# Performance work log

Hardware: AMD Instinct MI355X
Metric: run time of the kernel (lower is better)

The kernel has to match this reference:

```python
import jax, jax.numpy as jnp
import numpy as np

C = 128          # hidden_channels
N = 50000        # num nodes
E = 600000       # num edges
G = 256          # num graphs
PI = 3.141592653589793
EPS = 1e-5       # BatchNorm eps


def _lin(key, fan_in, fan_out):
    return jax.random.normal(key, (fan_in, fan_out), jnp.float32) / jnp.sqrt(fan_in)


def setup_inputs() -> dict:
    key = jax.random.key(0)
    ks = jax.random.split(key, 40)
    inp = {}
    inp["x"] = jax.random.normal(ks[0], (N, C), jnp.float32)
    inp["edge_index"] = jax.random.randint(ks[1], (2, E), 0, N)
    inp["edge_attr"] = jax.random.normal(ks[2], (E, C), jnp.float32)
    inp["batch"] = jnp.sort(jax.random.randint(ks[3], (N,), 0, G))
    # GATv2Conv 1
    inp["Wl1"] = _lin(ks[4], C, C); inp["bl1"] = jnp.zeros((C,), jnp.float32)
    inp["Wr1"] = _lin(ks[5], C, C); inp["br1"] = jnp.zeros((C,), jnp.float32)
    inp["We1"] = _lin(ks[6], C, C)
    inp["att1"] = jax.random.normal(ks[7], (C,), jnp.float32) / jnp.sqrt(C)
    inp["bo1"] = jnp.zeros((C,), jnp.float32)
    # GATv2Conv 2
    inp["Wl2"] = _lin(ks[8], C, C); inp["bl2"] = jnp.zeros((C,), jnp.float32)
    inp["Wr2"] = _lin(ks[9], C, C); inp["br2"] = jnp.zeros((C,), jnp.float32)
    inp["We2"] = _lin(ks[10], C, C)
    inp["att2"] = jax.random.normal(ks[11], (C,), jnp.float32) / jnp.sqrt(C)
    inp["bo2"] = jnp.zeros((C,), jnp.float32)
    # BatchNorms (affine)
    inp["g1"] = jnp.ones((C,), jnp.float32); inp["be1"] = jnp.zeros((C,), jnp.float32)
    inp["g2"] = jnp.ones((C,), jnp.float32); inp["be2"] = jnp.zeros((C,), jnp.float32)
    # AttentionalAggregation gate MLP (lin1 -> tanh -> lin2)
    inp["Ag1"] = _lin(ks[12], C, C); inp["bg1"] = jnp.zeros((C,), jnp.float32)
    inp["Ag2"] = _lin(ks[13], C, C); inp["bg2"] = jnp.zeros((C,), jnp.float32)
    # final Linear
    inp["Wf"] = _lin(ks[14], C, C); inp["bf"] = jnp.zeros((C,), jnp.float32)
    return inp


def gatv2(x, src, dst, ea, Wl, bl, Wr, br, We, att, bo):
    # add self-loops with fill_value='mean' (mean of incoming edge_attr per node)
    ones = jnp.ones(src.shape, x.dtype)
    deg = jax.ops.segment_sum(ones, dst, N)
    loop_attr = jax.ops.segment_sum(ea, dst, N) / jnp.maximum(deg, 1.0)[:, None]
    ar = jnp.arange(N)
    s = jnp.concatenate([src, ar])
    d = jnp.concatenate([dst, ar])
    ea_full = jnp.concatenate([ea, loop_attr], axis=0)  # [E+N, C]
    xl = x @ Wl + bl   # source transform
    xr = x @ Wr + br   # target transform
    m = xl[s] + xr[d] + ea_full @ We                    # [E+N, C]
    a = jnp.sum(jax.nn.leaky_relu(m, 0.2) * att, axis=-1)  # [E+N]
    # scatter-softmax over incoming edges of each target node
    amax = jax.ops.segment_max(a, d, N)
    ex = jnp.exp(a - amax[d])
    den = jax.ops.segment_sum(ex, d, N)
    alpha = ex / den[d]
    return jax.ops.segment_sum(alpha[:, None] * xl[s], d, N) + bo


def batchnorm(x, g, b):
    mu = x.mean(axis=0)
    var = x.var(axis=0)
    return (x - mu) * jax.lax.rsqrt(var + EPS) * g + b


def att_pool(x, batch, A1, b1, A2, b2):
    # gate_nn: lin1 -> tanh -> lin2, then per-graph per-feature softmax weights
    gate = jnp.tanh(x @ A1 + b1) @ A2 + b2              # [N, C]
    gmax = jax.ops.segment_max(gate, batch, G)
    eg = jnp.exp(gate - gmax[batch])
    den = jax.ops.segment_sum(eg, batch, G)
    w = eg / den[batch]
    return jax.ops.segment_sum(w * x, batch, G)          # [G, C]


def reference(x, edge_index, edge_attr, batch,
              Wl1, bl1, Wr1, br1, We1, att1, bo1,
              Wl2, bl2, Wr2, br2, We2, att2, bo2,
              g1, be1, g2, be2,
              Ag1, bg1, Ag2, bg2, Wf, bf):
    src, dst = edge_index[0], edge_index[1]
    h = gatv2(x, src, dst, edge_attr, Wl1, bl1, Wr1, br1, We1, att1, bo1)
    h = jnp.tanh(batchnorm(h, g1, be1))   # dropout = identity (eval)
    h = gatv2(h, src, dst, edge_attr, Wl2, bl2, Wr2, br2, We2, att2, bo2)
    h = jnp.tanh(batchnorm(h, g2, be2))
    p = att_pool(h, batch, Ag1, bg1, Ag2, bg2)           # [G, C]
    o = jnp.tanh(p @ Wf + bf)
    axis, aperture = jnp.split(o, 2, axis=-1)            # [G, C//2] each
    return axis * PI, (aperture + 1.0) * PI
```

## Files before the change

### kernel.cpp

```cpp
#include <hip/hip_runtime.h>
#include <hip/hip_bf16.h>
#include <math.h>

#define C 128
#define NN 50000
#define EE 600000
#define GG 256
#define PI_F 3.14159265358979323846f
#define EPS_BN 1e-5f

typedef __attribute__((ext_vector_type(8)))  short  short8;
typedef __attribute__((ext_vector_type(16))) float  floatx16;
typedef __attribute__((ext_vector_type(4)))  float  float4v;
typedef __attribute__((ext_vector_type(4)))  unsigned short ushort4v;

static __device__ __forceinline__ short f2bs(float x) {
    union { float f; unsigned u; } v; v.f = x;
    unsigned r = v.u + 0x7FFF + ((v.u >> 16) & 1);
    return (short)(r >> 16);
}
static __device__ __forceinline__ float bs2f(unsigned short b) {
    union { unsigned u; float f; } v; v.u = (unsigned)b << 16; return v.f;
}

__global__ void k_cast(const float* __restrict__ in, unsigned short* __restrict__ out, int n4) {
    int i = blockIdx.x * blockDim.x + threadIdx.x;
    if (i < n4) {
        float4v v = ((const float4v*)in)[i];
        ushort4v o;
        o.x = (unsigned short)f2bs(v.x); o.y = (unsigned short)f2bs(v.y);
        o.z = (unsigned short)f2bs(v.z); o.w = (unsigned short)f2bs(v.w);
        ((ushort4v*)out)[i] = o;
    }
}

__global__ void k_count(const int* __restrict__ dst, int* __restrict__ deg) {
    int e = blockIdx.x * blockDim.x + threadIdx.x;
    if (e < EE) atomicAdd(&deg[dst[e]], 1);
}

__global__ void k_scan(const int* __restrict__ deg, int* __restrict__ row_ptr) {
    __shared__ int s[1024];
    int t = threadIdx.x;
    const int CH = (NN + 1023) / 1024;
    int base = t * CH;
    int loc = 0;
    for (int i = 0; i < CH; i++) { int idx = base + i; if (idx < NN) loc += deg[idx]; }
    s[t] = loc; __syncthreads();
    for (int off = 1; off < 1024; off <<= 1) {
        int v = (t >= off) ? s[t - off] : 0;
        __syncthreads();
        s[t] += v;
        __syncthreads();
    }
    int run = (t == 0) ? 0 : s[t - 1];
    for (int i = 0; i < CH; i++) {
        int idx = base + i;
        if (idx < NN) { row_ptr[idx] = run; run += deg[idx]; }
    }
    if (t == 0) row_ptr[NN] = s[1023];
}

__global__ void k_fill(const int* __restrict__ src, const int* __restrict__ dst,
                       const int* __restrict__ row_ptr, int* __restrict__ fill,
                       int* __restrict__ eid, int* __restrict__ scsr, int* __restrict__ dcsr) {
    int e = blockIdx.x * blockDim.x + threadIdx.x;
    if (e < EE) {
        int d = dst[e];
        int pos = atomicAdd(&fill[d], 1);
        int i = row_ptr[d] + pos;
        eid[i] = e;
        scsr[i] = src[e];
        dcsr[i] = d;
    }
}

__global__ void k_cast_perm(const float* __restrict__ ea, const int* __restrict__ eid,
                            unsigned short* __restrict__ out) {
    int i = blockIdx.x * 4 + (threadIdx.x >> 6);
    int lane = threadIdx.x & 63;
    if (i >= EE) return;
    int e = eid[i];
    const float2* rp = (const float2*)(ea + (size_t)e * C);
    float2 v = rp[lane];
    unsigned pk = (unsigned)(unsigned short)f2bs(v.x) | ((unsigned)(unsigned short)f2bs(v.y) << 16);
    ((unsigned*)(out + (size_t)i * C))[lane] = pk;
}

__global__ void k_esum(const unsigned short* __restrict__ ea_csr, const int* __restrict__ row_ptr,
                       unsigned short* __restrict__ esum) {
    int n = blockIdx.x; int c = threadIdx.x;
    int s = row_ptr[n], e = row_ptr[n + 1];
    float acc = 0.f;
    for (int i = s; i < e; i++) acc += bs2f(ea_csr[(size_t)i * C + c]);
    esum[(size_t)n * C + c] = (unsigned short)f2bs(acc / fmaxf((float)(e - s), 1.f));
}

template<bool TANH, bool OUT_BF16>
__launch_bounds__(256)
__global__ void k_gemm(const unsigned short* __restrict__ A, const float* __restrict__ W,
                       const float* __restrict__ bias, void* __restrict__ outv, int M) {
    __shared__ short sWT[C * 136];
    for (int i = threadIdx.x; i < C * C; i += 256) {
        int k = i >> 7, n = i & (C - 1);
        sWT[n * 136 + k] = f2bs(W[i]);
    }
    __syncthreads();

    int lane = threadIdx.x & 63;
    int wave = threadIdx.x >> 6;
    int m    = lane & 31;
    int half = lane >> 5;
    int row0 = blockIdx.x * 128 + wave * 32;
    int rowA = row0 + m;
    int rowC = (rowA < M) ? rowA : (M - 1);
    const unsigned short* rp = A + (size_t)rowC * C;

    floatx16 acc[4];
    #pragma unroll
    for (int t = 0; t < 4; ++t)
        #pragma unroll
        for (int r = 0; r < 16; ++r) acc[t][r] = 0.f;

    #pragma unroll
    for (int s = 0; s < 8; ++s) {
        int k0 = s * 16 + half * 8;
        short8 af = *(const short8*)(rp + k0);
        #pragma unroll
        for (int t = 0; t < 4; ++t) {
            short8 bfr = *(const short8*)(&sWT[(t * 32 + m) * 136 + k0]);
            acc[t] = __builtin_amdgcn_mfma_f32_32x32x16_bf16(af, bfr, acc[t], 0, 0, 0);
        }
    }

    #pragma unroll
    for (int t = 0; t < 4; ++t) {
        int n = t * 32 + m;
        float b = bias ? bias[n] : 0.f;
        #pragma unroll
        for (int r = 0; r < 16; ++r) {
            int rl  = (r & 3) + 8 * (r >> 2) + 4 * half;
            int row = row0 + rl;
            if (row < M) {
                float v = acc[t][r] + b;
                if (TANH) v = tanhf(v);
                if (OUT_BF16) ((unsigned short*)outv)[(size_t)row * C + n] = (unsigned short)f2bs(v);
                else          ((float*)outv)[(size_t)row * C + n] = v;
            }
        }
    }
}

__launch_bounds__(256)
__global__ void k_gemm2(const unsigned short* __restrict__ A,
                        const float* __restrict__ W0, const float* __restrict__ b0,
                        const float* __restrict__ W1, const float* __restrict__ b1,
                        unsigned short* __restrict__ out0, unsigned short* __restrict__ out1,
                        int M) {
    __shared__ short sWT[C * 136];
    int lane = threadIdx.x & 63;
    int wave = threadIdx.x >> 6;
    int m    = lane & 31;
    int half = lane >> 5;
    int row0 = blockIdx.x * 128 + wave * 32;
    int rowA = row0 + m;
    int rowC = (rowA < M) ? rowA : (M - 1);
    const unsigned short* rp = A + (size_t)rowC * C;

    short8 af[8];
    #pragma unroll
    for (int s = 0; s < 8; ++s) af[s] = *(const short8*)(rp + s * 16 + half * 8);

    for (int phase = 0; phase < 2; ++phase) {
        const float* W = phase ? W1 : W0;
        const float* bb = phase ? b1 : b0;
        unsigned short* out = phase ? out1 : out0;
        if (phase) __syncthreads();
        for (int i = threadIdx.x; i < C * C; i += 256) {
            int k = i >> 7, n = i & (C - 1);
            sWT[n * 136 + k] = f2bs(W[i]);
        }
        __syncthreads();

        floatx16 acc[4];
        #pragma unroll
        for (int t = 0; t < 4; ++t)
            #pragma unroll
            for (int r = 0; r < 16; ++r) acc[t][r] = 0.f;

        #pragma unroll
        for (int s = 0; s < 8; ++s) {
            int k0 = s * 16 + half * 8;
            #pragma unroll
            for (int t = 0; t < 4; ++t) {
                short8 bfr = *(const short8*)(&sWT[(t * 32 + m) * 136 + k0]);
                acc[t] = __builtin_amdgcn_mfma_f32_32x32x16_bf16(af[s], bfr, acc[t], 0, 0, 0);
            }
        }

        #pragma unroll
        for (int t = 0; t < 4; ++t) {
            int n = t * 32 + m;
            float b = bb[n];
            #pragma unroll
            for (int r = 0; r < 16; ++r) {
                int rl  = (r & 3) + 8 * (r >> 2) + 4 * half;
                int row = row0 + rl;
                if (row < M)
                    out[(size_t)row * C + n] = (unsigned short)f2bs(acc[t][r] + b);
            }
        }
    }
}

template<bool SELF>
__launch_bounds__(256)
__global__ void k_gemm_logit(const unsigned short* __restrict__ A, const float* __restrict__ W,
                             const unsigned short* __restrict__ xl, const unsigned short* __restrict__ xr,
                             const int* __restrict__ scsr, const int* __restrict__ dcsr,
                             const float* __restrict__ att, float* __restrict__ aout, int M) {
    __shared__ short sWT[C * 136];
    for (int i = threadIdx.x; i < C * C; i += 256) {
        int k = i >> 7, n = i & (C - 1);
        sWT[n * 136 + k] = f2bs(W[i]);
    }
    __syncthreads();

    int lane = threadIdx.x & 63;
    int wave = threadIdx.x >> 6;
    int m    = lane & 31;
    int half = lane >> 5;
    int row0 = blockIdx.x * 128 + wave * 32;
    int rowA = row0 + m;
    int rowC = (rowA < M) ? rowA : (M - 1);
    const unsigned short* rp = A + (size_t)rowC * C;

    floatx16 acc[4];
    #pragma unroll
    for (int t = 0; t < 4; ++t)
        #pragma unroll
        for (int r = 0; r < 16; ++r) acc[t][r] = 0.f;

    #pragma unroll
    for (int s = 0; s < 8; ++s) {
        int k0 = s * 16 + half * 8;
        short8 af = *(const short8*)(rp + k0);
        #pragma unroll
        for (int t = 0; t < 4; ++t) {
            short8 bfr = *(const short8*)(&sWT[(t * 32 + m) * 136 + k0]);
            acc[t] = __builtin_amdgcn_mfma_f32_32x32x16_bf16(af, bfr, acc[t], 0, 0, 0);
        }
    }

    float attv[4];
    #pragma unroll
    for (int t = 0; t < 4; ++t) attv[t] = att[t * 32 + m];

    #pragma unroll
    for (int r = 0; r < 16; ++r) {
        int rl  = (r & 3) + 8 * (r >> 2) + 4 * half;
        int row = row0 + rl;
        int rc  = (row < M) ? row : (M - 1);
        int si, di;
        if (SELF) { si = rc; di = rc; }
        else      { si = scsr[rc]; di = dcsr[rc]; }
        const unsigned short* xls = xl + (size_t)si * C;
        const unsigned short* xrs = xr + (size_t)di * C;
        float p = 0.f;
        #pragma unroll
        for (int t = 0; t < 4; ++t) {
            int col = t * 32 + m;
            float v = acc[t][r] + bs2f(xls[col]) + bs2f(xrs[col]);
            v = (v >= 0.f) ? v : 0.2f * v;
            p = fmaf(v, attv[t], p);
        }
        p += __shfl_xor(p, 1);  p += __shfl_xor(p, 2);  p += __shfl_xor(p, 4);
        p += __shfl_xor(p, 8);  p += __shfl_xor(p, 16);
        if (m == 0 && row < M) aout[row] = p;
    }
}

__global__ void k_attn(const unsigned short* __restrict__ xl, const float* __restrict__ a,
                       const int* __restrict__ row_ptr, const int* __restrict__ scsr,
                       const float* __restrict__ bo, float* __restrict__ out) {
    int n = blockIdx.x * 4 + (threadIdx.x >> 6);
    int lane = threadIdx.x & 63;
    if (n >= NN) return;
    int s = row_ptr[n], e = row_ptr[n + 1];
    float aself = a[EE + n];
    float mx = aself;
    for (int i = s + lane; i < e; i += 64) mx = fmaxf(mx, a[i]);
    #pragma unroll
    for (int o = 1; o < 64; o <<= 1) mx = fmaxf(mx, __shfl_xor(mx, o));
    float part = (lane == 0) ? expf(aself - mx) : 0.f;
    for (int i = s + lane; i < e; i += 64) part += expf(a[i] - mx);
    #pragma unroll
    for (int o = 1; o < 64; o <<= 1) part += __shfl_xor(part, o);
    float inv = 1.f / part;

    int sub = lane >> 4;
    int cb  = (lane & 15) * 8;
    float acc[8];
    #pragma unroll
    for (int j = 0; j < 8; ++j) acc[j] = 0.f;

    if (sub == 0) {
        float w = expf(aself - mx) * inv;
        short8 v = *(const short8*)(xl + (size_t)n * C + cb);
        #pragma unroll
        for (int j = 0; j < 8; ++j) acc[j] = w * bs2f((unsigned short)v[j]);
    }

    for (int i = s + sub; i < e; i += 4) {
        float w = expf(a[i] - mx) * inv;
        int sd = scsr[i];
        short8 v = *(const short8*)(xl + (size_t)sd * C + cb);
        #pragma unroll
        for (int j = 0; j < 8; ++j) acc[j] = fmaf(w, bs2f((unsigned short)v[j]), acc[j]);
    }

    #pragma unroll
    for (int j = 0; j < 8; ++j) {
        acc[j] += __shfl_xor(acc[j], 16);
        acc[j] += __shfl_xor(acc[j], 32);
    }
    if (sub == 0) {
        float* op = out + (size_t)n * C + cb;
        float4v o0, o1;
        o0.x = acc[0] + bo[cb + 0]; o0.y = acc[1] + bo[cb + 1];
        o0.z = acc[2] + bo[cb + 2]; o0.w = acc[3] + bo[cb + 3];
        o1.x = acc[4] + bo[cb + 4]; o1.y = acc[5] + bo[cb + 5];
        o1.z = acc[6] + bo[cb + 6]; o1.w = acc[7] + bo[cb + 7];
        ((float4v*)op)[0] = o0;
        ((float4v*)op)[1] = o1;
    }
}

__global__ void k_bnstats(const float* __restrict__ v, float* __restrict__ sums) {
    int c = threadIdx.x;
    float s1 = 0.f, s2 = 0.f;
    for (int n = blockIdx.x; n < NN; n += gridDim.x) {
        float x = v[(size_t)n * C + c]; s1 += x; s2 += x * x;
    }
    atomicAdd(&sums[c], s1); atomicAdd(&sums[C + c], s2);
}

__global__ void k_bnapply(const float* __restrict__ v, const float* __restrict__ sums,
                          const float* __restrict__ g, const float* __restrict__ b,
                          unsigned short* __restrict__ h) {
    int idx = blockIdx.x * blockDim.x + threadIdx.x;
    if (idx >= NN * C) return;
    int c = idx & (C - 1);
    float mu  = sums[c] * (1.f / NN);
    float var = sums[C + c] * (1.f / NN) - mu * mu;
    float r = rsqrtf(var + EPS_BN);
    h[idx] = (unsigned short)f2bs(tanhf((v[idx] - mu) * r * g[c] + b[c]));
}

__global__ void k_bounds(const int* __restrict__ batch, int* __restrict__ gs, int* __restrict__ ge) {
    int n = blockIdx.x * blockDim.x + threadIdx.x;
    if (n >= NN) return;
    int b = batch[n];
    if (n == 0 || batch[n - 1] != b) gs[b] = n;
    if (n == NN - 1 || batch[n + 1] != b) ge[b] = n + 1;
}

__global__ void k_pool(const unsigned short* __restrict__ gate, const unsigned short* __restrict__ h,
                       const int* __restrict__ gs, const int* __restrict__ ge,
                       float* __restrict__ pooled) {
    __shared__ float sm[C], sden[C], sacc[C];
    int g = blockIdx.x;
    int t = threadIdx.x;
    int c = t & (C - 1);
    int half = t >> 7;
    int s = gs[g], e = ge[g];
    float m = -1e30f, den = 0.f, acc = 0.f;
    for (int n = s + half; n < e; n += 2) {
        float gv = bs2f(gate[(size_t)n * C + c]);
        float hv = bs2f(h[(size_t)n * C + c]);
        float mn = fmaxf(m, gv);
        float sc = expf(m - mn);
        float w  = expf(gv - mn);
        den = den * sc + w;
        acc = acc * sc + w * hv;
        m = mn;
    }
    if (half) { sm[c] = m; sden[c] = den; sacc[c] = acc; }
    __syncthreads();
    if (!half) {
        float m2 = sm[c], den2 = sden[c], acc2 = sacc[c];
        float mn = fmaxf(m, m2);
        float a1 = expf(m - mn), a2 = expf(m2 - mn);
        float d  = den * a1 + den2 * a2;
        float ac = acc * a1 + acc2 * a2;
        pooled[g * C + c] = (e > s) ? ac / d : 0.f;
    }
}

__global__ void k_final(const float* __restrict__ pooled, const float* __restrict__ Wf,
                        const float* __restrict__ bf, float* __restrict__ out) {
    __shared__ float row[C];
    int g = blockIdx.x; int j = threadIdx.x;
    row[j] = pooled[g * C + j];
    __syncthreads();
    float acc = bf[j];
    #pragma unroll 8
    for (int k = 0; k < C; k++) acc = fmaf(row[k], Wf[k * C + j], acc);
    float o = tanhf(acc);
    if (j < C / 2) out[g * (C / 2) + j] = o * PI_F;
    else out[GG * (C / 2) + g * (C / 2) + (j - C / 2)] = (o + 1.f) * PI_F;
}

extern "C" void kernel_launch(void* const* d_in, const int* in_sizes, int n_in,
                              void* d_out, int out_size, void* d_ws, size_t ws_size,
                              hipStream_t stream) {
    const float* x   = (const float*)d_in[0];
    const int*   ei  = (const int*)d_in[1];
    const float* ea  = (const float*)d_in[2];
    const int* batch = (const int*)d_in[3];
    const float *Wl1 = (const float*)d_in[4],  *bl1 = (const float*)d_in[5];
    const float *Wr1 = (const float*)d_in[6],  *br1 = (const float*)d_in[7];
    const float *We1 = (const float*)d_in[8],  *att1 = (const float*)d_in[9], *bo1 = (const float*)d_in[10];
    const float *Wl2 = (const float*)d_in[11], *bl2 = (const float*)d_in[12];
    const float *Wr2 = (const float*)d_in[13], *br2 = (const float*)d_in[14];
    const float *We2 = (const float*)d_in[15], *att2 = (const float*)d_in[16], *bo2 = (const float*)d_in[17];
    const float *g1  = (const float*)d_in[18], *be1 = (const float*)d_in[19];
    const float *g2  = (const float*)d_in[20], *be2 = (const float*)d_in[21];
    const float *Ag1 = (const float*)d_in[22], *bg1 = (const float*)d_in[23];
    const float *Ag2 = (const float*)d_in[24], *bg2 = (const float*)d_in[25];
    const float *Wf  = (const float*)d_in[26], *bf  = (const float*)d_in[27];
    const int* src = ei; const int* dst = ei + EE;

    char* wsb = (char*)d_ws;
    size_t off = 0;
    auto alloc = [&](size_t bytes) -> char* {
        char* p = wsb + off; off += (bytes + 255) & ~(size_t)255; return p;
    };
    unsigned short* ea_u  = (unsigned short*)alloc((size_t)EE * C * 2);
    unsigned short* x_u   = (unsigned short*)alloc((size_t)NN * C * 2);
    unsigned short* xl_u  = (unsigned short*)alloc((size_t)NN * C * 2);
    unsigned short* xr_u  = (unsigned short*)alloc((size_t)NN * C * 2);
    unsigned short* h_u   = (unsigned short*)alloc((size_t)NN * C * 2);
    unsigned short* es_u  = (unsigned short*)alloc((size_t)NN * C * 2);
    float* aggf  = (float*)alloc((size_t)NN * C * 4);
    float* a     = (float*)alloc((size_t)(EE + NN) * 4);
    int*   csrz  = (int*)alloc((size_t)2 * NN * 4);
    int* deg = csrz, *fill = csrz + NN;
    int* row_ptr = (int*)alloc((size_t)(NN + 1) * 4);
    int* eid     = (int*)alloc((size_t)EE * 4);
    int* scsr    = (int*)alloc((size_t)EE * 4);
    int* dcsr    = (int*)alloc((size_t)EE * 4);
    float* sums  = (float*)alloc(4 * C * 4);
    int* gbounds = (int*)alloc(2 * GG * 4);
    int* gs = gbounds, *ge = gbounds + GG;
    float* pooled= (float*)alloc(GG * C * 4);

    hipMemsetAsync(csrz,    0, (size_t)2 * NN * 4, stream);
    hipMemsetAsync(sums,    0, 4 * C * 4, stream);
    hipMemsetAsync(gbounds, 0, 2 * GG * 4, stream);

    k_cast<<<(NN * C / 4 + 255) / 256, 256, 0, stream>>>(x, x_u, NN * C / 4);
    k_count<<<(EE + 255) / 256, 256, 0, stream>>>(dst, deg);
    k_scan<<<1, 1024, 0, stream>>>(deg, row_ptr);
    k_fill<<<(EE + 255) / 256, 256, 0, stream>>>(src, dst, row_ptr, fill, eid, scsr, dcsr);
    k_cast_perm<<<(EE + 3) / 4, 256, 0, stream>>>(ea, eid, ea_u);
    k_esum<<<NN, C, 0, stream>>>(ea_u, row_ptr, es_u);

    int gN = (NN + 127) / 128, gE = (EE + 127) / 128;

    k_gemm2<<<gN, 256, 0, stream>>>(x_u, Wl1, bl1, Wr1, br1, xl_u, xr_u, NN);
    k_gemm_logit<true ><<<gN, 256, 0, stream>>>(es_u, We1, xl_u, xr_u, nullptr, nullptr, att1, a + EE, NN);
    k_gemm_logit<false><<<gE, 256, 0, stream>>>(ea_u, We1, xl_u, xr_u, scsr, dcsr, att1, a, EE);
    k_attn<<<(NN + 3) / 4, 256, 0, stream>>>(xl_u, a, row_ptr, scsr, bo1, aggf);
    k_bnstats<<<256, C, 0, stream>>>(aggf, sums);
    k_bnapply<<<(NN * C + 255) / 256, 256, 0, stream>>>(aggf, sums, g1, be1, h_u);

    k_gemm2<<<gN, 256, 0, stream>>>(h_u, Wl2, bl2, Wr2, br2, xl_u, xr_u, NN);
    k_gemm_logit<true ><<<gN, 256, 0, stream>>>(es_u, We2, xl_u, xr_u, nullptr, nullptr, att2, a + EE, NN);
    k_gemm_logit<false><<<gE, 256, 0, stream>>>(ea_u, We2, xl_u, xr_u, scsr, dcsr, att2, a, EE);
    k_attn<<<(NN + 3) / 4, 256, 0, stream>>>(xl_u, a, row_ptr, scsr, bo2, aggf);
    k_bnstats<<<256, C, 0, stream>>>(aggf, sums + 2 * C);
    k_bnapply<<<(NN * C + 255) / 256, 256, 0, stream>>>(aggf, sums + 2 * C, g2, be2, h_u);

    k_gemm<true,  true><<<gN, 256, 0, stream>>>(h_u,  Ag1, bg1, xl_u, NN);
    k_gemm<false, true><<<gN, 256, 0, stream>>>(xl_u, Ag2, bg2, xr_u, NN);
    k_bounds<<<(NN + 255) / 256, 256, 0, stream>>>(batch, gs, ge);
    k_pool<<<GG, 256, 0, stream>>>(xr_u, h_u, gs, ge, pooled);
    k_final<<<GG, C, 0, stream>>>(pooled, Wf, bf, (float*)d_out);
}
```

Baseline: 1.394 ms.

## Pretranspose weights once, parallelize scan, fuse cast+esum and pool+final, widen BN kernels

Adds a prep kernel that converts and transposes all eight weight matrices to bf16 once, so each GEMM block only copies them into shared memory instead of converting fp32 weights per block. The single-block scan is replaced by a three-phase multi-block scan. The edge-attribute permute-cast and the per-node mean are fused into one kernel. The BN stats and pooling kernels use 1024 threads with shared-memory reductions, BN apply is vectorised by four, and pooling is fused with the final linear layer. The fused cast/esum reads fp32 edge rows in a strided per-node pattern, which may coalesce less well than the previous per-edge cast.

```diff
diff --git a/kernel.cpp b/kernel.cpp
--- a/kernel.cpp
+++ b/kernel.cpp
@@ -8,6 +8,7 @@
 #define GG 256
 #define PI_F 3.14159265358979323846f
 #define EPS_BN 1e-5f
+#define SCAN_G ((NN + 255) / 256)
 
 typedef __attribute__((ext_vector_type(8)))  short  short8;
 typedef __attribute__((ext_vector_type(16))) float  floatx16;
@@ -34,31 +35,87 @@
     }
 }
 
+__global__ void k_prep(const float* __restrict__ W0, const float* __restrict__ W1,
+                       const float* __restrict__ W2, const float* __restrict__ W3,
+                       const float* __restrict__ W4, const float* __restrict__ W5,
+                       const float* __restrict__ W6, const float* __restrict__ W7,
+                       unsigned short* __restrict__ WT) {
+    __shared__ short s[C * 136];
+    const float* W;
+    switch (blockIdx.x) {
+        case 0: W = W0; break; case 1: W = W1; break;
+        case 2: W = W2; break; case 3: W = W3; break;
+        case 4: W = W4; break; case 5: W = W5; break;
+        case 6: W = W6; break; default: W = W7; break;
+    }
+    for (int i = threadIdx.x; i < C * C; i += 256) {
+        int k = i >> 7, n = i & (C - 1);
+        s[n * 136 + k] = f2bs(W[i]);
+    }
+    __syncthreads();
+    unsigned short* out = WT + (size_t)blockIdx.x * C * C;
+    for (int i8 = threadIdx.x; i8 < C * C / 8; i8 += 256) {
+        int n = i8 >> 4, k0 = (i8 & 15) * 8;
+        *(short8*)(out + n * C + k0) = *(const short8*)&s[n * 136 + k0];
+    }
+}
+
+static __device__ __forceinline__ void stage_wt(const unsigned short* __restrict__ WT, short* sWT) {
+    for (int i8 = threadIdx.x; i8 < C * C / 8; i8 += 256) {
+        int n = i8 >> 4, k0 = (i8 & 15) * 8;
+        *(short8*)&sWT[n * 136 + k0] = *(const short8*)(WT + n * C + k0);
+    }
+}
+
 __global__ void k_count(const int* __restrict__ dst, int* __restrict__ deg) {
     int e = blockIdx.x * blockDim.x + threadIdx.x;
     if (e < EE) atomicAdd(&deg[dst[e]], 1);
 }
 
-__global__ void k_scan(const int* __restrict__ deg, int* __restrict__ row_ptr) {
-    __shared__ int s[1024];
+__global__ void k_scan1(const int* __restrict__ deg, int* __restrict__ bsum) {
+    __shared__ int s[256];
     int t = threadIdx.x;
-    const int CH = (NN + 1023) / 1024;
-    int base = t * CH;
-    int loc = 0;
-    for (int i = 0; i < CH; i++) { int idx = base + i; if (idx < NN) loc += deg[idx]; }
-    s[t] = loc; __syncthreads();
-    for (int off = 1; off < 1024; off <<= 1) {
+    int idx = blockIdx.x * 256 + t;
+    s[t] = (idx < NN) ? deg[idx] : 0;
+    __syncthreads();
+    for (int off = 128; off > 0; off >>= 1) {
+        if (t < off) s[t] += s[t + off];
+        __syncthreads();
+    }
+    if (t == 0) bsum[blockIdx.x] = s[0];
+}
+
+__global__ void k_scan2(const int* __restrict__ bsum, int* __restrict__ boff, int* __restrict__ row_ptr) {
+    __shared__ int s[256];
+    int t = threadIdx.x;
+    int v0 = (t < SCAN_G) ? bsum[t] : 0;
+    s[t] = v0;
+    __syncthreads();
+    for (int off = 1; off < 256; off <<= 1) {
         int v = (t >= off) ? s[t - off] : 0;
         __syncthreads();
         s[t] += v;
         __syncthreads();
     }
-    int run = (t == 0) ? 0 : s[t - 1];
-    for (int i = 0; i < CH; i++) {
-        int idx = base + i;
-        if (idx < NN) { row_ptr[idx] = run; run += deg[idx]; }
-    }
-    if (t == 0) row_ptr[NN] = s[1023];
+    if (t < SCAN_G) boff[t] = s[t] - v0;
+    if (t == 255) row_ptr[NN] = s[255];
+}
+
+__global__ void k_scan3(const int* __restrict__ deg, const int* __restrict__ boff,
+                        int* __restrict__ row_ptr) {
+    __shared__ int s[256];
+    int t = threadIdx.x;
+    int idx = blockIdx.x * 256 + t;
+    int v = (idx < NN) ? deg[idx] : 0;
+    s[t] = v;
+    __syncthreads();
+    for (int off = 1; off < 256; off <<= 1) {
+        int u = (t >= off) ? s[t - off] : 0;
+        __syncthreads();
+        s[t] += u;
+        __syncthreads();
+    }
+    if (idx < NN) row_ptr[idx] = boff[blockIdx.x] + s[t] - v;
 }
 
 __global__ void k_fill(const int* __restrict__ src, const int* __restrict__ dst,
@@ -75,36 +132,26 @@
     }
 }
 
-__global__ void k_cast_perm(const float* __restrict__ ea, const int* __restrict__ eid,
-                            unsigned short* __restrict__ out) {
-    int i = blockIdx.x * 4 + (threadIdx.x >> 6);
-    int lane = threadIdx.x & 63;
-    if (i >= EE) return;
-    int e = eid[i];
-    const float2* rp = (const float2*)(ea + (size_t)e * C);
-    float2 v = rp[lane];
-    unsigned pk = (unsigned)(unsigned short)f2bs(v.x) | ((unsigned)(unsigned short)f2bs(v.y) << 16);
-    ((unsigned*)(out + (size_t)i * C))[lane] = pk;
-}
-
-__global__ void k_esum(const unsigned short* __restrict__ ea_csr, const int* __restrict__ row_ptr,
-                       unsigned short* __restrict__ esum) {
+__global__ void k_cast_esum(const float* __restrict__ ea, const int* __restrict__ eid,
+                            const int* __restrict__ row_ptr,
+                            unsigned short* __restrict__ ea_csr, unsigned short* __restrict__ esum) {
     int n = blockIdx.x; int c = threadIdx.x;
     int s = row_ptr[n], e = row_ptr[n + 1];
     float acc = 0.f;
-    for (int i = s; i < e; i++) acc += bs2f(ea_csr[(size_t)i * C + c]);
+    for (int i = s; i < e; i++) {
+        float v = ea[(size_t)eid[i] * C + c];
+        acc += v;
+        ea_csr[(size_t)i * C + c] = (unsigned short)f2bs(v);
+    }
     esum[(size_t)n * C + c] = (unsigned short)f2bs(acc / fmaxf((float)(e - s), 1.f));
 }
 
 template<bool TANH, bool OUT_BF16>
 __launch_bounds__(256)
-__global__ void k_gemm(const unsigned short* __restrict__ A, const float* __restrict__ W,
+__global__ void k_gemm(const unsigned short* __restrict__ A, const unsigned short* __restrict__ WT,
                        const float* __restrict__ bias, void* __restrict__ outv, int M) {
     __shared__ short sWT[C * 136];
-    for (int i = threadIdx.x; i < C * C; i += 256) {
-        int k = i >> 7, n = i & (C - 1);
-        sWT[n * 136 + k] = f2bs(W[i]);
-    }
+    stage_wt(WT, sWT);
     __syncthreads();
 
     int lane = threadIdx.x & 63;
@@ -153,8 +200,8 @@
 
 __launch_bounds__(256)
 __global__ void k_gemm2(const unsigned short* __restrict__ A,
-                        const float* __restrict__ W0, const float* __restrict__ b0,
-                        const float* __restrict__ W1, const float* __restrict__ b1,
+                        const unsigned short* __restrict__ WT0, const float* __restrict__ b0,
+                        const unsigned short* __restrict__ WT1, const float* __restrict__ b1,
                         unsigned short* __restrict__ out0, unsigned short* __restrict__ out1,
                         int M) {
     __shared__ short sWT[C * 136];
@@ -172,14 +219,11 @@
     for (int s = 0; s < 8; ++s) af[s] = *(const short8*)(rp + s * 16 + half * 8);
 
     for (int phase = 0; phase < 2; ++phase) {
-        const float* W = phase ? W1 : W0;
+        const unsigned short* WT = phase ? WT1 : WT0;
         const float* bb = phase ? b1 : b0;
         unsigned short* out = phase ? out1 : out0;
         if (phase) __syncthreads();
-        for (int i = threadIdx.x; i < C * C; i += 256) {
-            int k = i >> 7, n = i & (C - 1);
-            sWT[n * 136 + k] = f2bs(W[i]);
-        }
+        stage_wt(WT, sWT);
         __syncthreads();
 
         floatx16 acc[4];
@@ -215,15 +259,12 @@
 
 template<bool SELF>
 __launch_bounds__(256)
-__global__ void k_gemm_logit(const unsigned short* __restrict__ A, const float* __restrict__ W,
+__global__ void k_gemm_logit(const unsigned short* __restrict__ A, const unsigned short* __restrict__ WT,
                              const unsigned short* __restrict__ xl, const unsigned short* __restrict__ xr,
                              const int* __restrict__ scsr, const int* __restrict__ dcsr,
                              const float* __restrict__ att, float* __restrict__ aout, int M) {
     __shared__ short sWT[C * 136];
-    for (int i = threadIdx.x; i < C * C; i += 256) {
-        int k = i >> 7, n = i & (C - 1);
-        sWT[n * 136 + k] = f2bs(W[i]);
-    }
+    stage_wt(WT, sWT);
     __syncthreads();
 
     int lane = threadIdx.x & 63;
@@ -336,25 +377,42 @@
     }
 }
 
+__launch_bounds__(1024)
 __global__ void k_bnstats(const float* __restrict__ v, float* __restrict__ sums) {
-    int c = threadIdx.x;
+    __shared__ float r1[8][C], r2[8][C];
+    int c = threadIdx.x & (C - 1);
+    int q = threadIdx.x >> 7;
     float s1 = 0.f, s2 = 0.f;
-    for (int n = blockIdx.x; n < NN; n += gridDim.x) {
+    for (int n = blockIdx.x * 8 + q; n < NN; n += 8 * gridDim.x) {
         float x = v[(size_t)n * C + c]; s1 += x; s2 += x * x;
     }
-    atomicAdd(&sums[c], s1); atomicAdd(&sums[C + c], s2);
+    r1[q][c] = s1; r2[q][c] = s2;
+    __syncthreads();
+    if (threadIdx.x < C) {
+        float a1 = 0.f, a2 = 0.f;
+        #pragma unroll
+        for (int k = 0; k < 8; ++k) { a1 += r1[k][c]; a2 += r2[k][c]; }
+        atomicAdd(&sums[c], a1); atomicAdd(&sums[C + c], a2);
+    }
 }
 
 __global__ void k_bnapply(const float* __restrict__ v, const float* __restrict__ sums,
                           const float* __restrict__ g, const float* __restrict__ b,
                           unsigned short* __restrict__ h) {
-    int idx = blockIdx.x * blockDim.x + threadIdx.x;
-    if (idx >= NN * C) return;
-    int c = idx & (C - 1);
-    float mu  = sums[c] * (1.f / NN);
-    float var = sums[C + c] * (1.f / NN) - mu * mu;
-    float r = rsqrtf(var + EPS_BN);
-    h[idx] = (unsigned short)f2bs(tanhf((v[idx] - mu) * r * g[c] + b[c]));
+    int i4 = blockIdx.x * blockDim.x + threadIdx.x;
+    if (i4 >= NN * C / 4) return;
+    int c0 = (i4 * 4) & (C - 1);
+    float4v x = ((const float4v*)v)[i4];
+    ushort4v o;
+    #pragma unroll
+    for (int j = 0; j < 4; ++j) {
+        int c = c0 + j;
+        float mu  = sums[c] * (1.f / NN);
+        float var = sums[C + c] * (1.f / NN) - mu * mu;
+        float r = rsqrtf(var + EPS_BN);
+        o[j] = (unsigned short)f2bs(tanhf((x[j] - mu) * r * g[c] + b[c]));
+    }
+    ((ushort4v*)h)[i4] = o;
 }
 
 __global__ void k_bounds(const int* __restrict__ batch, int* __restrict__ gs, int* __restrict__ ge) {
@@ -365,17 +423,20 @@
     if (n == NN - 1 || batch[n + 1] != b) ge[b] = n + 1;
 }
 
-__global__ void k_pool(const unsigned short* __restrict__ gate, const unsigned short* __restrict__ h,
-                       const int* __restrict__ gs, const int* __restrict__ ge,
-                       float* __restrict__ pooled) {
-    __shared__ float sm[C], sden[C], sacc[C];
+__launch_bounds__(1024)
+__global__ void k_poolfinal(const unsigned short* __restrict__ gate, const unsigned short* __restrict__ h,
+                            const int* __restrict__ gs, const int* __restrict__ ge,
+                            const float* __restrict__ Wf, const float* __restrict__ bf,
+                            float* __restrict__ out) {
+    __shared__ float sm[8][C], sden[8][C], sacc[8][C];
+    __shared__ float row[C];
     int g = blockIdx.x;
     int t = threadIdx.x;
     int c = t & (C - 1);
-    int half = t >> 7;
+    int q = t >> 7;
     int s = gs[g], e = ge[g];
     float m = -1e30f, den = 0.f, acc = 0.f;
-    for (int n = s + half; n < e; n += 2) {
+    for (int n = s + q; n < e; n += 8) {
         float gv = bs2f(gate[(size_t)n * C + c]);
         float hv = bs2f(h[(size_t)n * C + c]);
         float mn = fmaxf(m, gv);
@@ -385,30 +446,38 @@
         acc = acc * sc + w * hv;
         m = mn;
     }
-    if (half) { sm[c] = m; sden[c] = den; sacc[c] = acc; }
-    __syncthreads();
-    if (!half) {
-        float m2 = sm[c], den2 = sden[c], acc2 = sacc[c];
-        float mn = fmaxf(m, m2);
-        float a1 = expf(m - mn), a2 = expf(m2 - mn);
-        float d  = den * a1 + den2 * a2;
-        float ac = acc * a1 + acc2 * a2;
-        pooled[g * C + c] = (e > s) ? ac / d : 0.f;
-    }
-}
-
-__global__ void k_final(const float* __restrict__ pooled, const float* __restrict__ Wf,
-                        const float* __restrict__ bf, float* __restrict__ out) {
-    __shared__ float row[C];
-    int g = blockIdx.x; int j = threadIdx.x;
-    row[j] = pooled[g * C + j];
-    __syncthreads();
-    float acc = bf[j];
-    #pragma unroll 8
-    for (int k = 0; k < C; k++) acc = fmaf(row[k], Wf[k * C + j], acc);
-    float o = tanhf(acc);
-    if (j < C / 2) out[g * (C / 2) + j] = o * PI_F;
-    else out[GG * (C / 2) + g * (C / 2) + (j - C / 2)] = (o + 1.f) * PI_F;
+    sm[q][c] = m; sden[q][c] = den; sacc[q][c] = acc;
+    __syncthreads();
+    if (t < C) {
+        float M = sm[0][c];
+        #pragma unroll
+        for (int k = 1; k < 8; ++k) M = fmaxf(M, sm[k][c]);
+        float D = 0.f, A = 0.f;
+        #pragma unroll
+        for (int k = 0; k < 8; ++k) {
+            float al = expf(sm[k][c] - M);
+            D += sden[k][c] * al;
+            A += sacc[k][c] * al;
+        }
+        row[c] = (e > s) ? A / D : 0.f;
+    }
+    __syncthreads();
+    float p = 0.f;
+    #pragma unroll
+    for (int kk = 0; kk < 16; ++kk) {
+        int k = q * 16 + kk;
+        p = fmaf(row[k], Wf[k * C + c], p);
+    }
+    sden[q][c] = p;
+    __syncthreads();
+    if (t < C) {
+        float accf = bf[c];
+        #pragma unroll
+        for (int k = 0; k < 8; ++k) accf += sden[k][c];
+        float o = tanhf(accf);
+        if (c < C / 2) out[g * (C / 2) + c] = o * PI_F;
+        else out[GG * (C / 2) + g * (C / 2) + (c - C / 2)] = (o + 1.f) * PI_F;
+    }
 }
 
 extern "C" void kernel_launch(void* const* d_in, const int* in_sizes, int n_in,
@@ -442,6 +511,7 @@
     unsigned short* xr_u  = (unsigned short*)alloc((size_t)NN * C * 2);
     unsigned short* h_u   = (unsigned short*)alloc((size_t)NN * C * 2);
     unsigned short* es_u  = (unsigned short*)alloc((size_t)NN * C * 2);
+    unsigned short* WTall = (unsigned short*)alloc((size_t)8 * C * C * 2);
     float* aggf  = (float*)alloc((size_t)NN * C * 4);
     float* a     = (float*)alloc((size_t)(EE + NN) * 4);
     int*   csrz  = (int*)alloc((size_t)2 * NN * 4);
@@ -453,38 +523,45 @@
     float* sums  = (float*)alloc(4 * C * 4);
     int* gbounds = (int*)alloc(2 * GG * 4);
     int* gs = gbounds, *ge = gbounds + GG;
-    float* pooled= (float*)alloc(GG * C * 4);
+    int* bscan   = (int*)alloc((size_t)2 * SCAN_G * 4);
+    int* bsum = bscan, *boff = bscan + SCAN_G;
 
     hipMemsetAsync(csrz,    0, (size_t)2 * NN * 4, stream);
     hipMemsetAsync(sums,    0, 4 * C * 4, stream);
     hipMemsetAsync(gbounds, 0, 2 * GG * 4, stream);
 
+    const size_t WSZ = (size_t)C * C;
+    const unsigned short *WTl1 = WTall + 0 * WSZ, *WTr1 = WTall + 1 * WSZ, *WTe1 = WTall + 2 * WSZ;
+    const unsigned short *WTl2 = WTall + 3 * WSZ, *WTr2 = WTall + 4 * WSZ, *WTe2 = WTall + 5 * WSZ;
+    const unsigned short *WTA1 = WTall + 6 * WSZ, *WTA2 = WTall + 7 * WSZ;
+
+    k_prep<<<8, 256, 0, stream>>>(Wl1, Wr1, We1, Wl2, Wr2, We2, Ag1, Ag2, WTall);
     k_cast<<<(NN * C / 4 + 255) / 256, 256, 0, stream>>>(x, x_u, NN * C / 4);
     k_count<<<(EE + 255) / 256, 256, 0, stream>>>(dst, deg);
-    k_scan<<<1, 1024, 0, stream>>>(deg, row_ptr);
+    k_scan1<<<SCAN_G, 256, 0, stream>>>(deg, bsum);
+    k_scan2<<<1, 256, 0, stream>>>(bsum, boff, row_ptr);
+    k_scan3<<<SCAN_G, 256, 0, stream>>>(deg, boff, row_ptr);
     k_fill<<<(EE + 255) / 256, 256, 0, stream>>>(src, dst, row_ptr, fill, eid, scsr, dcsr);
-    k_cast_perm<<<(EE + 3) / 4, 256, 0, stream>>>(ea, eid, ea_u);
-    k_esum<<<NN, C, 0, stream>>>(ea_u, row_ptr, es_u);
+    k_cast_esum<<<NN, C, 0, stream>>>(ea, eid, row_ptr, ea_u, es_u);
 
     int gN = (NN + 127) / 128, gE = (EE + 127) / 128;
 
-    k_gemm2<<<gN, 256, 0, stream>>>(x_u, Wl1, bl1, Wr1, br1, xl_u, xr_u, NN);
-    k_gemm_logit<true ><<<gN, 256, 0, stream>>>(es_u, We1, xl_u, xr_u, nullptr, nullptr, att1, a + EE, NN);
-    k_gemm_logit<false><<<gE, 256, 0, stream>>>(ea_u, We1, xl_u, xr_u, scsr, dcsr, att1, a, EE);
+    k_gemm2<<<gN, 256, 0, stream>>>(x_u, WTl1, bl1, WTr1, br1, xl_u, xr_u, NN);
+    k_gemm_logit<true ><<<gN, 256, 0, stream>>>(es_u, WTe1, xl_u, xr_u, nullptr, nullptr, att1, a + EE, NN);
+    k_gemm_logit<false><<<gE, 256, 0, stream>>>(ea_u, WTe1, xl_u, xr_u, scsr, dcsr, att1, a, EE);
     k_attn<<<(NN + 3) / 4, 256, 0, stream>>>(xl_u, a, row_ptr, scsr, bo1, aggf);
-    k_bnstats<<<256, C, 0, stream>>>(aggf, sums);
-    k_bnapply<<<(NN * C + 255) / 256, 256, 0, stream>>>(aggf, sums, g1, be1, h_u);
-
-    k_gemm2<<<gN, 256, 0, stream>>>(h_u, Wl2, bl2, Wr2, br2, xl_u, xr_u, NN);
-    k_gemm_logit<true ><<<gN, 256, 0, stream>>>(es_u, We2, xl_u, xr_u, nullptr, nullptr, att2, a + EE, NN);
-    k_gemm_logit<false><<<gE, 256, 0, stream>>>(ea_u, We2, xl_u, xr_u, scsr, dcsr, att2, a, EE);
+    k_bnstats<<<256, 1024, 0, stream>>>(aggf, sums);
+    k_bnapply<<<(NN * C / 4 + 255) / 256, 256, 0, stream>>>(aggf, sums, g1, be1, h_u);
+
+    k_gemm2<<<gN, 256, 0, stream>>>(h_u, WTl2, bl2, WTr2, br2, xl_u, xr_u, NN);
+    k_gemm_logit<true ><<<gN, 256, 0, stream>>>(es_u, WTe2, xl_u, xr_u, nullptr, nullptr, att2, a + EE, NN);
+    k_gemm_logit<false><<<gE, 256, 0, stream>>>(ea_u, WTe2, xl_u, xr_u, scsr, dcsr, att2, a, EE);
     k_attn<<<(NN + 3) / 4, 256, 0, stream>>>(xl_u, a, row_ptr, scsr, bo2, aggf);
-    k_bnstats<<<256, C, 0, stream>>>(aggf, sums + 2 * C);
-    k_bnapply<<<(NN * C + 255) / 256, 256, 0, stream>>>(aggf, sums + 2 * C, g2, be2, h_u);
-
-    k_gemm<true,  true><<<gN, 256, 0, stream>>>(h_u,  Ag1, bg1, xl_u, NN);
-    k_gemm<false, true><<<gN, 256, 0, stream>>>(xl_u, Ag2, bg2, xr_u, NN);
+    k_bnstats<<<256, 1024, 0, stream>>>(aggf, sums + 2 * C);
+    k_bnapply<<<(NN * C / 4 + 255) / 256, 256, 0, stream>>>(aggf, sums + 2 * C, g2, be2, h_u);
+
+    k_gemm<true,  true><<<gN, 256, 0, stream>>>(h_u,  WTA1, bg1, xl_u, NN);
+    k_gemm<false, true><<<gN, 256, 0, stream>>>(xl_u, WTA2, bg2, xr_u, NN);
     k_bounds<<<(NN + 255) / 256, 256, 0, stream>>>(batch, gs, ge);
-    k_pool<<<GG, 256, 0, stream>>>(xr_u, h_u, gs, ge, pooled);
-    k_final<<<GG, C, 0, stream>>>(pooled, Wf, bf, (float*)d_out);
-}
+    k_poolfinal<<<GG, 1024, 0, stream>>>(xr_u, h_u, gs, ge, Wf, bf, (float*)d_out);
+}
```

Result: faster. 1.131 ms (-18.8%).
